# Optimization experiments

Hardware: AMD Instinct MI355X
Metric: run time of the kernel (lower is better)

## Reference

```python
import jax, jax.numpy as jnp
import numpy as np

B, N, T, H, W = 4, 256, 4096, 6, 8
SIM_DIM, LOOKUP, OUT_DIM = 128, 101, 128


def setup_inputs() -> dict:
    key = jax.random.key(0)
    k1, k2, k3, k4 = jax.random.split(key, 4)
    x = jax.random.normal(k1, (B, N, T, H, W), dtype=jnp.float32)
    # nn.Linear weights: [out_features, in_features]
    w_proj = jax.random.normal(k2, (SIM_DIM, N), dtype=jnp.float32) * (1.0 / np.sqrt(N))
    w_fc = jax.random.normal(k3, (OUT_DIM, LOOKUP), dtype=jnp.float32) * (1.0 / np.sqrt(LOOKUP))
    b_fc = jax.random.normal(k4, (OUT_DIM,), dtype=jnp.float32) * 0.01
    return {"x": x, "w_proj": w_proj, "w_fc": w_fc, "b_fc": b_fc}


def reference(x, w_proj, w_fc, b_fc):
    # x: [B, N, T, H, W] == torch.stack(inputs, dim=1) for N branch features
    pad = (LOOKUP - 1) // 2
    feat = x.mean(axis=(3, 4))                    # [B, N, T]  spatial mean-pool
    feat = jnp.swapaxes(feat, 1, 2)               # [B, T, N]
    proj = feat @ w_proj.T                        # [B, T, D]  projection (no bias)
    norm = jnp.linalg.norm(proj, axis=2, keepdims=True)
    proj = proj / jnp.maximum(norm, 1e-12)        # F.normalize(p=2, dim=2)
    sims = jnp.einsum('btd,bsd->bts', proj, proj)  # [B, T, T] full pairwise cosine sims
    sims_pad = jnp.pad(sims, ((0, 0), (0, 0), (pad, pad)))  # [B, T, T+w-1]
    # banded gather: band[b,t,j] = sims_pad[b, t, t + j]
    band_idx = jnp.arange(T)[:, None] + jnp.arange(LOOKUP)[None, :]  # [T, w]
    band = jnp.take_along_axis(sims_pad, band_idx[None], axis=2)     # [B, T, w]
    return jax.nn.relu(band @ w_fc.T + b_fc)      # [B, T, OUT_DIM]
```

## Files before the change

kernel.cpp:

```cpp
#include <hip/hip_runtime.h>

#define BB   4
#define NN   256
#define TT   4096
#define DD   128
#define LK   101
#define PADK 50
#define OD   128
#define ROWS 164
#define RSTR 33
#define FS_STR 68
#define WB_STR 132

typedef float vfloat4 __attribute__((ext_vector_type(4)));

__global__ __launch_bounds__(256) void transpose_w_kernel(
    const float* __restrict__ w_proj, const float* __restrict__ w_fc,
    float* __restrict__ w_t, float* __restrict__ wfc_t) {
  int idx = blockIdx.x * 256 + threadIdx.x;
  int stride = gridDim.x * 256;
  for (int i = idx; i < DD * NN; i += stride) {
    int d = i / NN, n = i - d * NN;
    w_t[n * DD + d] = w_proj[i];
  }
  for (int i = idx; i < OD * LK; i += stride) {
    int o = i / LK, j = i - o * LK;
    wfc_t[j * OD + o] = w_fc[i];
  }
}

__global__ __launch_bounds__(256) void pool_kernel(
    const float* __restrict__ x, float* __restrict__ feat) {
  __shared__ float part[512 * 13];
  int tid = threadIdx.x;
  const vfloat4* x4 = (const vfloat4*)x + (size_t)blockIdx.x * 6144;

  vfloat4 v[24];
#pragma unroll
  for (int k = 0; k < 24; ++k)
    v[k] = __builtin_nontemporal_load(&x4[tid + 256 * k]);

#pragma unroll
  for (int k = 0; k < 24; ++k) {
    int j = tid + 256 * k;
    int r = j / 12, i = j - r * 12;
    part[r * 13 + i] = (v[k].x + v[k].y) + (v[k].z + v[k].w);
  }
  __syncthreads();

  float* fo = feat + (size_t)blockIdx.x * 512;
#pragma unroll
  for (int q = 0; q < 2; ++q) {
    int o = tid + q * 256;
    const float* pp = part + o * 13;
    float a0 = 0.f, a1 = 0.f;
#pragma unroll
    for (int i = 0; i < 6; ++i) { a0 += pp[i]; a1 += pp[6 + i]; }
    fo[o] = (a0 + a1) * (1.0f / 48.0f);
  }
}

__global__ __launch_bounds__(512, 1) void proj_kernel(
    const float* __restrict__ feat, const float* __restrict__ w_t,
    float* __restrict__ projn) {
  extern __shared__ float smemP[];
  float* fs   = smemP;
  float* wbuf = smemP + NN * FS_STR;
  int b = blockIdx.x >> 6;
  int t0 = (blockIdx.x & 63) << 6;
  int tid = threadIdx.x;
  int td = tid & 31, tt = tid >> 5;

  float acc[4][4];
#pragma unroll
  for (int i = 0; i < 4; ++i)
#pragma unroll
    for (int j = 0; j < 4; ++j) acc[i][j] = 0.f;

  for (int c = 0; c < 4; ++c) {
    if (c) __syncthreads();
#pragma unroll
    for (int k = 0; k < 4; ++k) {
      int slot = tid + k * 512;
      int n = slot >> 5, d4 = slot & 31;
      *(float4*)(wbuf + n * WB_STR + d4 * 4) =
          *(const float4*)(w_t + (size_t)(c * 64 + n) * DD + d4 * 4);
    }
    if (c == 0) {
#pragma unroll
      for (int k = 0; k < 8; ++k) {
        int slot = tid + k * 512;
        int n = slot >> 4, t4 = slot & 15;
        *(float4*)(fs + n * FS_STR + t4 * 4) =
            *(const float4*)(feat + ((size_t)(b * NN + n)) * TT + t0 + t4 * 4);
      }
    }
    __syncthreads();

    const float* fp = fs + (c * 64) * FS_STR + tt * 4;
    const float* wp = wbuf + td * 4;
#pragma unroll 4
    for (int n = 0; n < 64; ++n) {
      float4 f = *(const float4*)(fp + n * FS_STR);
      float4 wv = *(const float4*)(wp + n * WB_STR);
      float fa[4] = {f.x, f.y, f.z, f.w};
#pragma unroll
      for (int i = 0; i < 4; ++i) {
        acc[i][0] += fa[i] * wv.x;
        acc[i][1] += fa[i] * wv.y;
        acc[i][2] += fa[i] * wv.z;
        acc[i][3] += fa[i] * wv.w;
      }
    }
  }

  float s[4];
#pragma unroll
  for (int i = 0; i < 4; ++i)
    s[i] = acc[i][0] * acc[i][0] + acc[i][1] * acc[i][1] +
           acc[i][2] * acc[i][2] + acc[i][3] * acc[i][3];
#pragma unroll
  for (int m = 1; m < 32; m <<= 1) {
#pragma unroll
    for (int i = 0; i < 4; ++i) s[i] += __shfl_xor(s[i], m, 64);
  }
#pragma unroll
  for (int i = 0; i < 4; ++i) {
    float inv = 1.0f / fmaxf(sqrtf(s[i]), 1e-12f);
    float4 o;
    o.x = acc[i][0] * inv; o.y = acc[i][1] * inv;
    o.z = acc[i][2] * inv; o.w = acc[i][3] * inv;
    *(float4*)(projn + ((size_t)(b * TT + t0 + tt * 4 + i)) * DD + td * 4) = o;
  }
}

__global__ __launch_bounds__(512, 1) void band_fc_kernel(
    const float* __restrict__ projn, const float* __restrict__ wfc_t,
    const float* __restrict__ b_fc, float* __restrict__ out) {
  extern __shared__ float4 smemC[];
  float4* p4 = smemC;
  float* band = (float*)(smemC + ROWS * RSTR);
  int b = blockIdx.x >> 6;
  int t0 = (blockIdx.x & 63) << 6;
  int tid = threadIdx.x;

  const float4* pg = (const float4*)projn;
  for (int i = tid; i < ROWS * 32; i += 512) {
    int r = i >> 5, c = i & 31;
    int t = t0 + r - PADK;
    float4 v = make_float4(0.f, 0.f, 0.f, 0.f);
    if (t >= 0 && t < TT) v = pg[(((size_t)b * TT + t) << 5) + c];
    p4[r * RSTR + c] = v;
  }
  __syncthreads();

  int w = tid >> 6, tt = tid & 63;

  float4 own[32];
#pragma unroll
  for (int c = 0; c < 32; ++c) own[c] = p4[(tt + PADK) * RSTR + c];

  int s0 = w * 21;
  int sEnd = (s0 + 21 < ROWS) ? (s0 + 21) : ROWS;
  for (int s = s0; s < sEnd; ++s) {
    float a0 = 0.f, a1 = 0.f, a2 = 0.f, a3 = 0.f;
#pragma unroll
    for (int c = 0; c < 32; ++c) {
      float4 ov = p4[s * RSTR + c];
      a0 += own[c].x * ov.x;
      a1 += own[c].y * ov.y;
      a2 += own[c].z * ov.z;
      a3 += own[c].w * ov.w;
    }
    int j = s - tt;
    if (j >= 0 && j < LK) band[tt * LK + j] = (a0 + a1) + (a2 + a3);
  }
  __syncthreads();

  int o0u = __builtin_amdgcn_readfirstlane((tid >> 6) * 16);
  float acc[16];
  const float4* bf4 = (const float4*)(b_fc + o0u);
#pragma unroll
  for (int k = 0; k < 4; ++k) {
    float4 bv = bf4[k];
    acc[4 * k + 0] = bv.x; acc[4 * k + 1] = bv.y;
    acc[4 * k + 2] = bv.z; acc[4 * k + 3] = bv.w;
  }
#pragma unroll 2
  for (int j = 0; j < LK; ++j) {
    float bv = band[tt * LK + j];
    const float4* wr = (const float4*)(wfc_t + j * OD + o0u);
#pragma unroll
    for (int k = 0; k < 4; ++k) {
      float4 wv = wr[k];
      acc[4 * k + 0] += wv.x * bv;
      acc[4 * k + 1] += wv.y * bv;
      acc[4 * k + 2] += wv.z * bv;
      acc[4 * k + 3] += wv.w * bv;
    }
  }
  float4* og = (float4*)(out + ((size_t)(b * TT + t0 + tt)) * OD + o0u);
#pragma unroll
  for (int k = 0; k < 4; ++k) {
    float4 o;
    o.x = fmaxf(acc[4 * k + 0], 0.f);
    o.y = fmaxf(acc[4 * k + 1], 0.f);
    o.z = fmaxf(acc[4 * k + 2], 0.f);
    o.w = fmaxf(acc[4 * k + 3], 0.f);
    og[k] = o;
  }
}

extern "C" void kernel_launch(void* const* d_in, const int* in_sizes, int n_in,
                              void* d_out, int out_size, void* d_ws, size_t ws_size,
                              hipStream_t stream) {
  const float* x      = (const float*)d_in[0];
  const float* w_proj = (const float*)d_in[1];
  const float* w_fc   = (const float*)d_in[2];
  const float* b_fc   = (const float*)d_in[3];
  float* out = (float*)d_out;

  char* ws = (char*)d_ws;
  float* feat  = (float*)ws;
  float* projn = (float*)(ws + 16777216);
  float* w_t   = (float*)(ws + 16777216 + 8388608);
  float* wfc_t = (float*)(ws + 16777216 + 8388608 + 131072);

  size_t smP = (size_t)(NN * FS_STR + 64 * WB_STR) * sizeof(float);
  size_t smC = (size_t)ROWS * RSTR * sizeof(float4) + (size_t)64 * LK * sizeof(float);
  (void)hipFuncSetAttribute((const void*)proj_kernel,
                      hipFuncAttributeMaxDynamicSharedMemorySize, (int)smP);
  (void)hipFuncSetAttribute((const void*)band_fc_kernel,
                      hipFuncAttributeMaxDynamicSharedMemorySize, (int)smC);

  transpose_w_kernel<<<64, 256, 0, stream>>>(w_proj, w_fc, w_t, wfc_t);
  pool_kernel<<<(BB * NN * TT) / 512, 256, 0, stream>>>(x, feat);
  proj_kernel<<<BB * (TT / 64), 512, smP, stream>>>(feat, w_t, projn);
  band_fc_kernel<<<BB * (TT / 64), 512, smC, stream>>>(projn, wfc_t, b_fc, out);
}
```

Measured before the change: 215.4 us.

## Use fp16 packed dot2 for banded similarity and raise band kernel occupancy

The band kernel now stores the normalized projection tile in shared memory as packed fp16 pairs and computes the pairwise similarities with fdot2 instructions, which halves LDS footprint and traffic and the instruction count of the dot products. Each thread loads and converts its own row straight from global memory into fp16 registers. Launch bounds are raised to allow several blocks per CU. The pool kernel also drops its nontemporal loads. The fp16 rounding of the unit vectors introduces a small precision loss in the similarity values.

```diff
diff --git a/kernel.cpp b/kernel.cpp
--- a/kernel.cpp
+++ b/kernel.cpp
@@ -8,11 +8,27 @@
 #define PADK 50
 #define OD   128
 #define ROWS 164
-#define RSTR 33
+#define P16W 68
 #define FS_STR 68
 #define WB_STR 132
 
 typedef float vfloat4 __attribute__((ext_vector_type(4)));
+typedef unsigned int vuint4 __attribute__((ext_vector_type(4)));
+typedef _Float16 half2v __attribute__((ext_vector_type(2)));
+
+__device__ inline float fdot2f(half2v a, half2v b, float c) {
+#if __has_builtin(__builtin_amdgcn_fdot2)
+  return __builtin_amdgcn_fdot2(a, b, c, false);
+#else
+  return c + (float)a.x * (float)b.x + (float)a.y * (float)b.y;
+#endif
+}
+__device__ inline unsigned int pk16(float lo, float hi) {
+  return __builtin_bit_cast(unsigned int, __builtin_amdgcn_cvt_pkrtz(lo, hi));
+}
+__device__ inline half2v h2(unsigned int u) {
+  return __builtin_bit_cast(half2v, u);
+}
 
 __global__ __launch_bounds__(256) void transpose_w_kernel(
     const float* __restrict__ w_proj, const float* __restrict__ w_fc,
@@ -38,7 +54,7 @@
   vfloat4 v[24];
 #pragma unroll
   for (int k = 0; k < 24; ++k)
-    v[k] = __builtin_nontemporal_load(&x4[tid + 256 * k]);
+    v[k] = x4[tid + 256 * k];
 
 #pragma unroll
   for (int k = 0; k < 24; ++k) {
@@ -134,43 +150,55 @@
   }
 }
 
-__global__ __launch_bounds__(512, 1) void band_fc_kernel(
+__global__ __launch_bounds__(512, 4) void band_fc_kernel(
     const float* __restrict__ projn, const float* __restrict__ wfc_t,
     const float* __restrict__ b_fc, float* __restrict__ out) {
-  extern __shared__ float4 smemC[];
-  float4* p4 = smemC;
-  float* band = (float*)(smemC + ROWS * RSTR);
+  extern __shared__ unsigned int smemF[];
+  unsigned int* p16 = smemF;
+  float* band = (float*)(smemF + ROWS * P16W);
   int b = blockIdx.x >> 6;
   int t0 = (blockIdx.x & 63) << 6;
   int tid = threadIdx.x;
+  int w = tid >> 6, tt = tid & 63;
 
   const float4* pg = (const float4*)projn;
   for (int i = tid; i < ROWS * 32; i += 512) {
     int r = i >> 5, c = i & 31;
     int t = t0 + r - PADK;
-    float4 v = make_float4(0.f, 0.f, 0.f, 0.f);
-    if (t >= 0 && t < TT) v = pg[(((size_t)b * TT + t) << 5) + c];
-    p4[r * RSTR + c] = v;
+    unsigned int w0 = 0, w1 = 0;
+    if (t >= 0 && t < TT) {
+      float4 v = pg[(((size_t)b * TT + t) << 5) + c];
+      w0 = pk16(v.x, v.y);
+      w1 = pk16(v.z, v.w);
+    }
+    p16[r * P16W + c * 2] = w0;
+    p16[r * P16W + c * 2 + 1] = w1;
+  }
+
+  half2v own2[64];
+  {
+    const float4* orow = (const float4*)(projn + ((size_t)(b * TT + t0 + tt)) * DD);
+#pragma unroll
+    for (int c = 0; c < 32; ++c) {
+      float4 v = orow[c];
+      own2[2 * c]     = h2(pk16(v.x, v.y));
+      own2[2 * c + 1] = h2(pk16(v.z, v.w));
+    }
   }
   __syncthreads();
-
-  int w = tid >> 6, tt = tid & 63;
-
-  float4 own[32];
-#pragma unroll
-  for (int c = 0; c < 32; ++c) own[c] = p4[(tt + PADK) * RSTR + c];
 
   int s0 = w * 21;
   int sEnd = (s0 + 21 < ROWS) ? (s0 + 21) : ROWS;
   for (int s = s0; s < sEnd; ++s) {
+    const vuint4* ps = (const vuint4*)(p16 + s * P16W);
     float a0 = 0.f, a1 = 0.f, a2 = 0.f, a3 = 0.f;
 #pragma unroll
-    for (int c = 0; c < 32; ++c) {
-      float4 ov = p4[s * RSTR + c];
-      a0 += own[c].x * ov.x;
-      a1 += own[c].y * ov.y;
-      a2 += own[c].z * ov.z;
-      a3 += own[c].w * ov.w;
+    for (int c = 0; c < 16; ++c) {
+      vuint4 v = ps[c];
+      a0 = fdot2f(own2[c * 4 + 0], h2(v.x), a0);
+      a1 = fdot2f(own2[c * 4 + 1], h2(v.y), a1);
+      a2 = fdot2f(own2[c * 4 + 2], h2(v.z), a2);
+      a3 = fdot2f(own2[c * 4 + 3], h2(v.w), a3);
     }
     int j = s - tt;
     if (j >= 0 && j < LK) band[tt * LK + j] = (a0 + a1) + (a2 + a3);
@@ -227,14 +255,14 @@
   float* wfc_t = (float*)(ws + 16777216 + 8388608 + 131072);
 
   size_t smP = (size_t)(NN * FS_STR + 64 * WB_STR) * sizeof(float);
-  size_t smC = (size_t)ROWS * RSTR * sizeof(float4) + (size_t)64 * LK * sizeof(float);
+  size_t smF = (size_t)ROWS * P16W * sizeof(int) + (size_t)64 * LK * sizeof(float);
   (void)hipFuncSetAttribute((const void*)proj_kernel,
                       hipFuncAttributeMaxDynamicSharedMemorySize, (int)smP);
   (void)hipFuncSetAttribute((const void*)band_fc_kernel,
-                      hipFuncAttributeMaxDynamicSharedMemorySize, (int)smC);
+                      hipFuncAttributeMaxDynamicSharedMemorySize, (int)smF);
 
   transpose_w_kernel<<<64, 256, 0, stream>>>(w_proj, w_fc, w_t, wfc_t);
   pool_kernel<<<(BB * NN * TT) / 512, 256, 0, stream>>>(x, feat);
   proj_kernel<<<BB * (TT / 64), 512, smP, stream>>>(feat, w_t, projn);
-  band_fc_kernel<<<BB * (TT / 64), 512, smC, stream>>>(projn, wfc_t, b_fc, out);
-}
+  band_fc_kernel<<<BB * (TT / 64), 512, smF, stream>>>(projn, wfc_t, b_fc, out);
+}
```

Result: slower. 240.0 us (+11.4%).
